# Kernel optimization log

Measured on AMD Instinct MI355X. Metric: run time of the kernel, lower is better.

Reference implementation:

```python
import jax, jax.numpy as jnp
import numpy as np

GROUP_SIZE = 64
IN_F, OUT_F, RANK = 4096, 4096, 32
N_TOKENS = 4096
N_GROUPS = IN_F // GROUP_SIZE


def setup_inputs() -> dict:
    key = jax.random.key(0)
    k = jax.random.split(key, 6)
    x = jax.random.normal(k[0], (N_TOKENS, IN_F), dtype=jnp.float32)
    # signed int4 values in [-8, 7], stored unpacked as int32
    main_qweight = jax.random.randint(k[1], (OUT_F, N_GROUPS, GROUP_SIZE), -8, 8, dtype=jnp.int32)
    main_wscale = jax.random.uniform(k[2], (OUT_F, N_GROUPS), dtype=jnp.float32) * 0.02 + 1e-3
    bias = jax.random.normal(k[3], (OUT_F,), dtype=jnp.float32) * 0.02
    proj_down_dense = jax.random.normal(k[4], (IN_F, RANK), dtype=jnp.float32) * 0.02
    proj_up_dense = jax.random.normal(k[5], (RANK, OUT_F), dtype=jnp.float32) * 0.02
    return {
        "x": x,
        "main_qweight": main_qweight,
        "main_wscale": main_wscale,
        "bias": bias,
        "proj_down_dense": proj_down_dense,
        "proj_up_dense": proj_up_dense,
    }


def reference(x, main_qweight, main_wscale, bias, proj_down_dense, proj_up_dense):
    n = x.shape[0]
    # --- per-group int8 activation quantization (symmetric, max-abs/127) ---
    xg = x.reshape(n, N_GROUPS, GROUP_SIZE).astype(jnp.float32)  # [N, G, gs]
    max_abs = jnp.max(jnp.abs(xg), axis=-1, keepdims=True)
    ascale = jnp.where(max_abs > 0, max_abs * (1.0 / 127.0), jnp.ones_like(max_abs))
    qx = jnp.clip(jnp.round(xg / ascale), -127.0, 127.0)
    # Fold per-group activation scales back in; per (out, group) weight scales into weight.
    # out[n,o] = sum_g ascale[n,g] * wscale[o,g] * sum_k qx[n,g,k] * qw[o,g,k]
    a_deq = (qx * ascale).reshape(n, IN_F)                                   # [N, in]
    w_deq = (main_qweight.astype(jnp.float32) * main_wscale[..., None]).reshape(OUT_F, IN_F)  # [out, in]
    out = a_deq @ w_deq.T + bias.astype(jnp.float32)                          # [N, out], fp32 accumulate
    # --- SVD low-rank correction: x @ proj_down @ proj_up (down in x dtype, up in fp32) ---
    low_rank = x @ proj_down_dense                                            # [N, rank]
    out = out + low_rank.astype(jnp.float32) @ proj_up_dense.astype(jnp.float32)
    return out.astype(x.dtype)
```

## Files before the change

### kernel.cpp

```cpp
#include <hip/hip_runtime.h>
#include <hip/hip_bf16.h>

#define IN_F  4096
#define OUT_F 4096
#define NTOK  4096
#define RANK  32
#define GS    64
#define NG    64
#define KTOT  4224
#define NKT   66
#define ITERS 33
#define KCH   1024

typedef __attribute__((ext_vector_type(4))) float f32x4;
typedef __attribute__((ext_vector_type(8))) short bf16x8;

#define AS1 __attribute__((address_space(1)))
#define AS3 __attribute__((address_space(3)))

__device__ __forceinline__ ushort f2bf(float f) {
  union { float f; uint u; } c; c.f = f;
  const uint u = c.u;
  return (ushort)((u + 0x7fffu + ((u >> 16) & 1u)) >> 16);
}

__global__ __launch_bounds__(256)
void prep_kernel(const float* __restrict__ x, const int* __restrict__ qw,
                 const float* __restrict__ wsc, const float* __restrict__ pd,
                 const float* __restrict__ pu, ushort* __restrict__ Aext,
                 ushort* __restrict__ Bext, ushort* __restrict__ pdT)
{
  const int bid = blockIdx.x;
  if (bid < 16384) {
    const int tid  = threadIdx.x;
    const int wave = tid >> 6, lane = tid & 63;
    const int sub  = lane & 15;
    const int ggrp = bid * 16 + wave * 4 + (lane >> 4);
    const int row  = ggrp >> 6, g = ggrp & 63;

    const float4 v = *(const float4*)(x + (size_t)row * IN_F + g * GS + sub * 4);
    float m = fmaxf(fmaxf(fabsf(v.x), fabsf(v.y)), fmaxf(fabsf(v.z), fabsf(v.w)));
    m = fmaxf(m, __shfl_xor(m, 1));
    m = fmaxf(m, __shfl_xor(m, 2));
    m = fmaxf(m, __shfl_xor(m, 4));
    m = fmaxf(m, __shfl_xor(m, 8));
    const float ascale = (m > 0.f) ? m * (1.f / 127.f) : 1.f;

    const float d0 = fminf(fmaxf(rintf(v.x / ascale), -127.f), 127.f) * ascale;
    const float d1 = fminf(fmaxf(rintf(v.y / ascale), -127.f), 127.f) * ascale;
    const float d2 = fminf(fmaxf(rintf(v.z / ascale), -127.f), 127.f) * ascale;
    const float d3 = fminf(fmaxf(rintf(v.w / ascale), -127.f), 127.f) * ascale;

    uint2 st;
    st.x = (uint)f2bf(d0) | ((uint)f2bf(d1) << 16);
    st.y = (uint)f2bf(d2) | ((uint)f2bf(d3) << 16);
    *(uint2*)(Aext + (size_t)row * KTOT + g * GS + sub * 4) = st;
  } else if (bid < 24576) {
    const int gidx = (bid - 16384) * 256 + threadIdx.x;
    const int o  = gidx >> 9;
    const int i0 = (gidx & 511) << 3;
    const float sc = wsc[o * NG + (i0 >> 6)];
    const int4 qa = *(const int4*)(qw + (size_t)o * IN_F + i0);
    const int4 qb = *(const int4*)(qw + (size_t)o * IN_F + i0 + 4);
    uint4 st;
    st.x = (uint)f2bf(qa.x * sc) | ((uint)f2bf(qa.y * sc) << 16);
    st.y = (uint)f2bf(qa.z * sc) | ((uint)f2bf(qa.w * sc) << 16);
    st.z = (uint)f2bf(qb.x * sc) | ((uint)f2bf(qb.y * sc) << 16);
    st.w = (uint)f2bf(qb.z * sc) | ((uint)f2bf(qb.w * sc) << 16);
    *(uint4*)(Bext + (size_t)o * KTOT + i0) = st;
  } else {
    const int id = (bid - 24576) * 256 + threadIdx.x;
    ushort* dst = Bext + (size_t)id * KTOT + IN_F;
    #pragma unroll
    for (int r = 0; r < RANK; ++r) {
      dst[r]            = f2bf(pu[(size_t)r * OUT_F + id]);
      dst[RANK + r]     = 0;
      dst[2 * RANK + r] = 0;
      dst[3 * RANK + r] = 0;
    }
    #pragma unroll
    for (int r = 0; r < RANK; ++r)
      pdT[(size_t)r * IN_F + id] = f2bf(pd[(size_t)id * RANK + r]);
  }
}

__global__ __launch_bounds__(256)
void lr_kernel(const ushort* __restrict__ A, const ushort* __restrict__ pdT,
               float* __restrict__ part)
{
  __shared__ alignas(16) ushort lA[64 * 64];
  const int tid  = threadIdx.x;
  const int wave = tid >> 6, lane = tid & 63;
  const int mt = blockIdx.x >> 2;
  const int kc = blockIdx.x & 3;
  const int k0 = kc * KCH;

  const int tr  = tid >> 3;
  const int scc = (tid & 7) ^ (tr & 7);
  const ushort* aSrc = A + (size_t)(mt * 64 + tr) * KTOT + k0 + scc * 8;
  char* ldsA = (char*)lA + wave * 1024;

  f32x4 acc[2];
  #pragma unroll
  for (int n = 0; n < 2; ++n) acc[n] = f32x4{0.f, 0.f, 0.f, 0.f};

  for (int kt = 0; kt < KCH / 64; ++kt) {
    const ushort* aS = aSrc + kt * 64;
    #pragma unroll
    for (int j = 0; j < 2; ++j)
      __builtin_amdgcn_global_load_lds(
          (const AS1 void*)(aS + (size_t)j * 32 * KTOT),
          (AS3 void*)(ldsA + j * 4096), 16, 0, 0);
    __syncthreads();
    #pragma unroll
    for (int ks = 0; ks < 2; ++ks) {
      const int kb  = (ks * 32 + (lane >> 4) * 8) * 2;
      const int row = wave * 16 + (lane & 15);
      const int addr = (row * 128 + kb) ^ ((row & 7) << 4);
      bf16x8 af = *(const bf16x8*)((const char*)lA + addr);
      #pragma unroll
      for (int n = 0; n < 2; ++n) {
        const int prow = n * 16 + (lane & 15);
        bf16x8 bf = *(const bf16x8*)(pdT + (size_t)prow * IN_F + k0 + kt * 64 + ks * 32 + (lane >> 4) * 8);
        acc[n] = __builtin_amdgcn_mfma_f32_16x16x32_bf16(af, bf, acc[n], 0, 0, 0);
      }
    }
    __syncthreads();
  }
  const int r0   = lane & 15;
  const int rowb = mt * 64 + wave * 16 + (lane >> 4) * 4;
  #pragma unroll
  for (int n = 0; n < 2; ++n)
    #pragma unroll
    for (int i = 0; i < 4; ++i)
      part[((size_t)kc * 4096 + rowb + i) * 32 + n * 16 + r0] = acc[n][i];
}

__global__ __launch_bounds__(256)
void lrcomb_kernel(const float* __restrict__ part, ushort* __restrict__ Aext)
{
  const int id  = blockIdx.x * 256 + threadIdx.x;
  const int row = id >> 5, r = id & 31;
  const float s = part[(size_t)row * 32 + r]
                + part[(size_t)(4096 + row) * 32 + r]
                + part[(size_t)(8192 + row) * 32 + r]
                + part[(size_t)(12288 + row) * 32 + r];
  ushort* dst = Aext + (size_t)row * KTOT + IN_F;
  dst[r]            = f2bf(s);
  dst[RANK + r]     = 0;
  dst[2 * RANK + r] = 0;
  dst[3 * RANK + r] = 0;
}

#define READ_AF8(DST, B_, MQ_)                                                   \
  { _Pragma("unroll")                                                            \
    for (int mf = 0; mf < 4; ++mf) {                                             \
      DST[mf][0] = *(const bf16x8*)(lds + afB0 + ((B_) * 32768 + (MQ_) * 8192 + mf * 2048)); \
      DST[mf][1] = *(const bf16x8*)(lds + afB1 + ((B_) * 32768 + (MQ_) * 8192 + mf * 2048)); \
    } }

#define READ_BF4(DST, B_, NQ_)                                                   \
  { _Pragma("unroll")                                                            \
    for (int nf = 0; nf < 2; ++nf) {                                             \
      DST[nf][0] = *(const bf16x8*)(lds + bfB0 + ((B_) * 32768 + (NQ_) * 4096 + nf * 2048)); \
      DST[nf][1] = *(const bf16x8*)(lds + bfB1 + ((B_) * 32768 + (NQ_) * 4096 + nf * 2048)); \
    } }

#define MFMA16(MQ_, NQ_, AF, BF)                                                 \
  _Pragma("unroll")                                                              \
  for (int mf = 0; mf < 4; ++mf)                                                 \
    _Pragma("unroll")                                                            \
    for (int nf = 0; nf < 2; ++nf)                                               \
      _Pragma("unroll")                                                          \
      for (int ks = 0; ks < 2; ++ks)                                             \
        acc[(MQ_) * 4 + mf][(NQ_) * 2 + nf] =                                    \
            __builtin_amdgcn_mfma_f32_16x16x32_bf16(AF[mf][ks], BF[nf][ks],      \
                acc[(MQ_) * 4 + mf][(NQ_) * 2 + nf], 0, 0, 0);

#define STAGE_A(B_, S0, S1, D0, D1, T_)                                          \
  { const ushort* s0 = Atile + S0 + (T_) * 64;                                   \
    const ushort* s1 = Atile + S1 + (T_) * 64;                                   \
    __builtin_amdgcn_global_load_lds((const AS1 void*)s0,                        \
        (AS3 void*)(lds + (B_) * 32768 + D0), 16, 0, 0);                         \
    __builtin_amdgcn_global_load_lds((const AS1 void*)s1,                        \
        (AS3 void*)(lds + (B_) * 32768 + D1), 16, 0, 0); }

#define STAGE_B(B_, S0, S1, D0, D1, T_)                                          \
  { const ushort* s0 = Btile + S0 + (T_) * 64;                                   \
    const ushort* s1 = Btile + S1 + (T_) * 64;                                   \
    __builtin_amdgcn_global_load_lds((const AS1 void*)s0,                        \
        (AS3 void*)(lds + 65536 + (B_) * 32768 + D0), 16, 0, 0);                 \
    __builtin_amdgcn_global_load_lds((const AS1 void*)s1,                        \
        (AS3 void*)(lds + 65536 + (B_) * 32768 + D1), 16, 0, 0); }

#define BAR __builtin_amdgcn_s_barrier()
#define DRAIN4 asm volatile("s_waitcnt vmcnt(4)" ::: "memory")
#define PRIO1 __builtin_amdgcn_s_setprio(1)
#define PRIO0 __builtin_amdgcn_s_setprio(0)

__global__ __launch_bounds__(512, 2)
void gemm256_kernel(const ushort* __restrict__ A, const ushort* __restrict__ B,
                    const float* __restrict__ bias, float* __restrict__ C)
{
  extern __shared__ char lds[];
  const int tid = threadIdx.x;
  const int w = tid >> 6, lane = tid & 63;
  const int l15 = lane & 15;
  const int wm = w >> 2, wn = w & 3;

  const int swz0 = (l15 * 128 + (lane >> 4) * 16) ^ ((l15 & 7) << 4);
  const int swz1 = (l15 * 128 + 64 + (lane >> 4) * 16) ^ ((l15 & 7) << 4);
  const int afB0 = wm * 16384 + swz0;
  const int afB1 = wm * 16384 + swz1;
  const int bfB0 = 65536 + wn * 8192 + swz0;
  const int bfB1 = 65536 + wn * 8192 + swz1;

  const int coff = ((lane & 7) ^ (lane >> 3)) << 3;
  const int g0 = w * 2, g1 = w * 2 + 1;
  const int aq0 = (g0 >> 3) * 2, asub0 = g0 & 7;
  const int aq1 = (g1 >> 3) * 2, asub1 = g1 & 7;
  const int aS00 = (aq0 * 64 + asub0 * 8 + (lane >> 3)) * KTOT + coff;
  const int aS01 = (aq1 * 64 + asub1 * 8 + (lane >> 3)) * KTOT + coff;
  const int aS10 = ((aq0 + 1) * 64 + asub0 * 8 + (lane >> 3)) * KTOT + coff;
  const int aS11 = ((aq1 + 1) * 64 + asub1 * 8 + (lane >> 3)) * KTOT + coff;
  const int aD00 = aq0 * 8192 + asub0 * 1024;
  const int aD01 = aq1 * 8192 + asub1 * 1024;
  const int aD10 = (aq0 + 1) * 8192 + asub0 * 1024;
  const int aD11 = (aq1 + 1) * 8192 + asub1 * 1024;
  const int bj0 = g0 >> 2, bsub0 = g0 & 3;
  const int bj1 = g1 >> 2, bsub1 = g1 & 3;
  const int bS00 = (bj0 * 64 + bsub0 * 8 + (lane >> 3)) * KTOT + coff;
  const int bS01 = (bj1 * 64 + bsub1 * 8 + (lane >> 3)) * KTOT + coff;
  const int bS10 = (bj0 * 64 + 32 + bsub0 * 8 + (lane >> 3)) * KTOT + coff;
  const int bS11 = (bj1 * 64 + 32 + bsub1 * 8 + (lane >> 3)) * KTOT + coff;
  const int bD00 = bj0 * 8192 + bsub0 * 1024;
  const int bD01 = bj1 * 8192 + bsub1 * 1024;
  const int bD10 = bj0 * 8192 + 4096 + bsub0 * 1024;
  const int bD11 = bj1 * 8192 + 4096 + bsub1 * 1024;

  const int xcd = blockIdx.x & 7, idx = blockIdx.x >> 3;
  const int bm = (xcd >> 1) * 4 + (idx >> 3);
  const int bn = (xcd & 1) * 8 + (idx & 7);

  const ushort* Atile = A + (size_t)bm * 256 * KTOT;
  const ushort* Btile = B + (size_t)bn * 256 * KTOT;

  f32x4 acc[8][4];
  #pragma unroll
  for (int m = 0; m < 8; ++m)
    #pragma unroll
    for (int n = 0; n < 4; ++n)
      acc[m][n] = f32x4{0.f, 0.f, 0.f, 0.f};

  bf16x8 afA[4][2], af2[4][2], b0[2][2], b1[2][2];

  STAGE_A(0, aS00, aS01, aD00, aD01, 0);
  STAGE_B(0, bS00, bS01, bD00, bD01, 0);
  STAGE_A(0, aS10, aS11, aD10, aD11, 0);
  STAGE_B(0, bS10, bS11, bD10, bD11, 0);
  STAGE_A(1, aS00, aS01, aD00, aD01, 1);
  STAGE_B(1, bS00, bS01, bD00, bD01, 1);
  DRAIN4;
  BAR;

  #pragma unroll 1
  for (int j = 0; j < ITERS; ++j) {
    const int t1 = 2 * j + 1;
    const int t2 = (2 * j + 2 < NKT) ? 2 * j + 2 : NKT - 1;
    const int t3 = (2 * j + 3 < NKT) ? 2 * j + 3 : NKT - 1;

    READ_AF8(afA, 0, 0);
    READ_BF4(b0, 0, 0);
    READ_BF4(b1, 0, 1);
    STAGE_A(1, aS10, aS11, aD10, aD11, t1);
    STAGE_B(1, bS10, bS11, bD10, bD11, t1);
    BAR;
    PRIO1; MFMA16(0, 0, afA, b0); MFMA16(0, 1, afA, b1); PRIO0;
    BAR;
    READ_AF8(af2, 0, 1);
    STAGE_A(0, aS00, aS01, aD00, aD01, t2);
    STAGE_B(0, bS00, bS01, bD00, bD01, t2);
    BAR;
    PRIO1; MFMA16(1, 0, af2, b0); MFMA16(1, 1, af2, b1); PRIO0;
    DRAIN4;
    BAR;
    READ_AF8(afA, 1, 0);
    READ_BF4(b0, 1, 0);
    READ_BF4(b1, 1, 1);
    STAGE_A(0, aS10, aS11, aD10, aD11, t2);
    STAGE_B(0, bS10, bS11, bD10, bD11, t2);
    BAR;
    PRIO1; MFMA16(0, 0, afA, b0); MFMA16(0, 1, afA, b1); PRIO0;
    BAR;
    READ_AF8(af2, 1, 1);
    STAGE_A(1, aS00, aS01, aD00, aD01, t3);
    STAGE_B(1, bS00, bS01, bD00, bD01, t3);
    BAR;
    PRIO1; MFMA16(1, 0, af2, b0); MFMA16(1, 1, af2, b1); PRIO0;
    DRAIN4;
    BAR;
  }

  const int csub = lane >> 4;
  #pragma unroll
  for (int nf = 0; nf < 4; ++nf) {
    const int col = bn * 256 + wn * 64 + nf * 16 + l15;
    const float bv = bias[col];
    #pragma unroll
    for (int mf = 0; mf < 8; ++mf) {
      const int row = bm * 256 + wm * 128 + mf * 16 + csub * 4;
      #pragma unroll
      for (int i = 0; i < 4; ++i)
        C[(size_t)(row + i) * OUT_F + col] = acc[mf][nf][i] + bv;
    }
  }
}

extern "C" void kernel_launch(void* const* d_in, const int* in_sizes, int n_in,
                              void* d_out, int out_size, void* d_ws, size_t ws_size,
                              hipStream_t stream) {
  const float* x    = (const float*)d_in[0];
  const int*   qw   = (const int*)d_in[1];
  const float* wsc  = (const float*)d_in[2];
  const float* bias = (const float*)d_in[3];
  const float* pd   = (const float*)d_in[4];
  const float* pu   = (const float*)d_in[5];
  float* out = (float*)d_out;

  ushort* Aext = (ushort*)d_ws;
  ushort* Bext = Aext + (size_t)NTOK * KTOT;
  ushort* pdT  = Bext + (size_t)OUT_F * KTOT;
  float*  part = (float*)(pdT + (size_t)RANK * IN_F);

  hipFuncSetAttribute(reinterpret_cast<const void*>(gemm256_kernel),
                      hipFuncAttributeMaxDynamicSharedMemorySize, 131072);

  prep_kernel  <<<24592, 256, 0, stream>>>(x, qw, wsc, pd, pu, Aext, Bext, pdT);
  lr_kernel    <<<  256, 256, 0, stream>>>(Aext, pdT, part);
  lrcomb_kernel<<<  512, 256, 0, stream>>>(part, Aext);
  gemm256_kernel<<< 256, 512, 131072, stream>>>(Aext, Bext, bias, out);
}
```

Measured before the change: 176.0 us.

## Switch GEMM to 32x32x16 MFMA and trim low-rank K padding

```diff
diff --git a/kernel.cpp b/kernel.cpp
--- a/kernel.cpp
+++ b/kernel.cpp
@@ -7,13 +7,14 @@
 #define RANK  32
 #define GS    64
 #define NG    64
-#define KTOT  4224
-#define NKT   66
-#define ITERS 33
+#define KTOT  4160
+#define NKT   65
+#define ITERS 32
 #define KCH   1024
 
-typedef __attribute__((ext_vector_type(4))) float f32x4;
-typedef __attribute__((ext_vector_type(8))) short bf16x8;
+typedef __attribute__((ext_vector_type(4)))  float f32x4;
+typedef __attribute__((ext_vector_type(16))) float f32x16;
+typedef __attribute__((ext_vector_type(8)))  short bf16x8;
 
 #define AS1 __attribute__((address_space(1)))
 #define AS3 __attribute__((address_space(3)))
@@ -73,10 +74,8 @@
     ushort* dst = Bext + (size_t)id * KTOT + IN_F;
     #pragma unroll
     for (int r = 0; r < RANK; ++r) {
-      dst[r]            = f2bf(pu[(size_t)r * OUT_F + id]);
-      dst[RANK + r]     = 0;
-      dst[2 * RANK + r] = 0;
-      dst[3 * RANK + r] = 0;
+      dst[r]        = f2bf(pu[(size_t)r * OUT_F + id]);
+      dst[RANK + r] = 0;
     }
     #pragma unroll
     for (int r = 0; r < RANK; ++r)
@@ -146,36 +145,32 @@
                 + part[(size_t)(8192 + row) * 32 + r]
                 + part[(size_t)(12288 + row) * 32 + r];
   ushort* dst = Aext + (size_t)row * KTOT + IN_F;
-  dst[r]            = f2bf(s);
-  dst[RANK + r]     = 0;
-  dst[2 * RANK + r] = 0;
-  dst[3 * RANK + r] = 0;
-}
-
-#define READ_AF8(DST, B_, MQ_)                                                   \
+  dst[r]        = f2bf(s);
+  dst[RANK + r] = 0;
+}
+
+#define READ_A(DST, B_, MQ_)                                                     \
   { _Pragma("unroll")                                                            \
-    for (int mf = 0; mf < 4; ++mf) {                                             \
-      DST[mf][0] = *(const bf16x8*)(lds + afB0 + ((B_) * 32768 + (MQ_) * 8192 + mf * 2048)); \
-      DST[mf][1] = *(const bf16x8*)(lds + afB1 + ((B_) * 32768 + (MQ_) * 8192 + mf * 2048)); \
+    for (int s = 0; s < 4; ++s) {                                                \
+      DST[0][s] = *(const bf16x8*)(lds + aB[s] + ((B_) * 32768 + (MQ_) * 8192)); \
+      DST[1][s] = *(const bf16x8*)(lds + aB[s] + ((B_) * 32768 + (MQ_) * 8192 + 4096)); \
     } }
 
-#define READ_BF4(DST, B_, NQ_)                                                   \
+#define READ_B(DST, B_, N_)                                                      \
   { _Pragma("unroll")                                                            \
-    for (int nf = 0; nf < 2; ++nf) {                                             \
-      DST[nf][0] = *(const bf16x8*)(lds + bfB0 + ((B_) * 32768 + (NQ_) * 4096 + nf * 2048)); \
-      DST[nf][1] = *(const bf16x8*)(lds + bfB1 + ((B_) * 32768 + (NQ_) * 4096 + nf * 2048)); \
-    } }
-
-#define MFMA16(MQ_, NQ_, AF, BF)                                                 \
+    for (int s = 0; s < 4; ++s)                                                  \
+      DST[s] = *(const bf16x8*)(lds + bB[s] + ((B_) * 32768 + (N_) * 4096)); }
+
+#define MFMA32(MQ_, AF, B0_, B1_)                                                \
   _Pragma("unroll")                                                              \
-  for (int mf = 0; mf < 4; ++mf)                                                 \
+  for (int s = 0; s < 4; ++s)                                                    \
     _Pragma("unroll")                                                            \
-    for (int nf = 0; nf < 2; ++nf)                                               \
-      _Pragma("unroll")                                                          \
-      for (int ks = 0; ks < 2; ++ks)                                             \
-        acc[(MQ_) * 4 + mf][(NQ_) * 2 + nf] =                                    \
-            __builtin_amdgcn_mfma_f32_16x16x32_bf16(AF[mf][ks], BF[nf][ks],      \
-                acc[(MQ_) * 4 + mf][(NQ_) * 2 + nf], 0, 0, 0);
+    for (int m2 = 0; m2 < 2; ++m2) {                                             \
+      acc[(MQ_) * 2 + m2][0] = __builtin_amdgcn_mfma_f32_32x32x16_bf16(          \
+          AF[m2][s], B0_[s], acc[(MQ_) * 2 + m2][0], 0, 0, 0);                   \
+      acc[(MQ_) * 2 + m2][1] = __builtin_amdgcn_mfma_f32_32x32x16_bf16(          \
+          AF[m2][s], B1_[s], acc[(MQ_) * 2 + m2][1], 0, 0, 0);                   \
+    }
 
 #define STAGE_A(B_, S0, S1, D0, D1, T_)                                          \
   { const ushort* s0 = Atile + S0 + (T_) * 64;                                   \
@@ -205,15 +200,18 @@
   extern __shared__ char lds[];
   const int tid = threadIdx.x;
   const int w = tid >> 6, lane = tid & 63;
-  const int l15 = lane & 15;
   const int wm = w >> 2, wn = w & 3;
-
-  const int swz0 = (l15 * 128 + (lane >> 4) * 16) ^ ((l15 & 7) << 4);
-  const int swz1 = (l15 * 128 + 64 + (lane >> 4) * 16) ^ ((l15 & 7) << 4);
-  const int afB0 = wm * 16384 + swz0;
-  const int afB1 = wm * 16384 + swz1;
-  const int bfB0 = 65536 + wn * 8192 + swz0;
-  const int bfB1 = 65536 + wn * 8192 + swz1;
+  const int L = lane & 31;
+  const int g16 = (lane >> 5) * 16;
+
+  int aB[4], bB[4];
+  #pragma unroll
+  for (int s = 0; s < 4; ++s) {
+    const int pre = L * 128 + s * 32 + g16;
+    const int sw  = pre ^ ((L & 7) << 4);
+    aB[s] = wm * 16384 + sw;
+    bB[s] = 65536 + wn * 8192 + sw;
+  }
 
   const int coff = ((lane & 7) ^ (lane >> 3)) << 3;
   const int g0 = w * 2, g1 = w * 2 + 1;
@@ -245,14 +243,16 @@
   const ushort* Atile = A + (size_t)bm * 256 * KTOT;
   const ushort* Btile = B + (size_t)bn * 256 * KTOT;
 
-  f32x4 acc[8][4];
-  #pragma unroll
-  for (int m = 0; m < 8; ++m)
-    #pragma unroll
-    for (int n = 0; n < 4; ++n)
-      acc[m][n] = f32x4{0.f, 0.f, 0.f, 0.f};
-
-  bf16x8 afA[4][2], af2[4][2], b0[2][2], b1[2][2];
+  f32x16 acc[4][2];
+  #pragma unroll
+  for (int m = 0; m < 4; ++m)
+    #pragma unroll
+    for (int n = 0; n < 2; ++n)
+      #pragma unroll
+      for (int r = 0; r < 16; ++r)
+        acc[m][n][r] = 0.f;
+
+  bf16x8 afA[2][4], af2[2][4], b0[4], b1[4];
 
   STAGE_A(0, aS00, aS01, aD00, aD01, 0);
   STAGE_B(0, bS00, bS01, bD00, bD01, 0);
@@ -269,49 +269,58 @@
     const int t2 = (2 * j + 2 < NKT) ? 2 * j + 2 : NKT - 1;
     const int t3 = (2 * j + 3 < NKT) ? 2 * j + 3 : NKT - 1;
 
-    READ_AF8(afA, 0, 0);
-    READ_BF4(b0, 0, 0);
-    READ_BF4(b1, 0, 1);
+    READ_A(afA, 0, 0);
+    READ_B(b0, 0, 0);
+    READ_B(b1, 0, 1);
     STAGE_A(1, aS10, aS11, aD10, aD11, t1);
     STAGE_B(1, bS10, bS11, bD10, bD11, t1);
     BAR;
-    PRIO1; MFMA16(0, 0, afA, b0); MFMA16(0, 1, afA, b1); PRIO0;
-    BAR;
-    READ_AF8(af2, 0, 1);
+    PRIO1; MFMA32(0, afA, b0, b1); PRIO0;
+    BAR;
+    READ_A(af2, 0, 1);
     STAGE_A(0, aS00, aS01, aD00, aD01, t2);
     STAGE_B(0, bS00, bS01, bD00, bD01, t2);
     BAR;
-    PRIO1; MFMA16(1, 0, af2, b0); MFMA16(1, 1, af2, b1); PRIO0;
+    PRIO1; MFMA32(1, af2, b0, b1); PRIO0;
     DRAIN4;
     BAR;
-    READ_AF8(afA, 1, 0);
-    READ_BF4(b0, 1, 0);
-    READ_BF4(b1, 1, 1);
+    READ_A(afA, 1, 0);
+    READ_B(b0, 1, 0);
+    READ_B(b1, 1, 1);
     STAGE_A(0, aS10, aS11, aD10, aD11, t2);
     STAGE_B(0, bS10, bS11, bD10, bD11, t2);
     BAR;
-    PRIO1; MFMA16(0, 0, afA, b0); MFMA16(0, 1, afA, b1); PRIO0;
-    BAR;
-    READ_AF8(af2, 1, 1);
+    PRIO1; MFMA32(0, afA, b0, b1); PRIO0;
+    BAR;
+    READ_A(af2, 1, 1);
     STAGE_A(1, aS00, aS01, aD00, aD01, t3);
     STAGE_B(1, bS00, bS01, bD00, bD01, t3);
     BAR;
-    PRIO1; MFMA16(1, 0, af2, b0); MFMA16(1, 1, af2, b1); PRIO0;
+    PRIO1; MFMA32(1, af2, b0, b1); PRIO0;
     DRAIN4;
     BAR;
   }
 
-  const int csub = lane >> 4;
-  #pragma unroll
-  for (int nf = 0; nf < 4; ++nf) {
-    const int col = bn * 256 + wn * 64 + nf * 16 + l15;
+  READ_A(afA, 0, 0);
+  READ_B(b0, 0, 0);
+  READ_B(b1, 0, 1);
+  MFMA32(0, afA, b0, b1);
+  READ_A(af2, 0, 1);
+  MFMA32(1, af2, b0, b1);
+
+  const int rofs = 4 * (lane >> 5);
+  #pragma unroll
+  for (int n = 0; n < 2; ++n) {
+    const int col = bn * 256 + wn * 64 + n * 32 + L;
     const float bv = bias[col];
     #pragma unroll
-    for (int mf = 0; mf < 8; ++mf) {
-      const int row = bm * 256 + wm * 128 + mf * 16 + csub * 4;
+    for (int m = 0; m < 4; ++m) {
+      const int rowb = bm * 256 + wm * 128 + m * 32 + rofs;
       #pragma unroll
-      for (int i = 0; i < 4; ++i)
-        C[(size_t)(row + i) * OUT_F + col] = acc[mf][nf][i] + bv;
+      for (int r = 0; r < 16; ++r) {
+        const int row = rowb + (r & 3) + 8 * (r >> 2);
+        C[(size_t)row * OUT_F + col] = acc[m][n][r] + bv;
+      }
     }
   }
 }
```

New measurement: 203.2 us. +15.5%, slower.
